# Performance work log

Measured on AMD Instinct MI355X. Metric: run time of the kernel, lower is better.

## Reference

```python
import jax, jax.numpy as jnp
import numpy as np

# model constants (match init_kwargs)
VOCAB = 32000
DIM = 1024
HEADS = 8
DH = DIM // HEADS
LAYERS = 2
K_SLOTS = 128
KR = 16   # read top-k
KW = 16   # write top-k
CHUNK = 256
GAMMA = 0.9  # slot memory decay per chunk


def setup_inputs() -> dict:
    key = jax.random.key(0)
    ks = jax.random.split(key, 12)
    B, S = 2, 4096
    s = 0.02
    inp = {
        "tokens": jax.random.randint(ks[0], (B, S), 0, VOCAB, dtype=jnp.int32),
        "embed": jax.random.normal(ks[1], (VOCAB, DIM), jnp.float32) * s,
        "Wq": jax.random.normal(ks[2], (LAYERS, DIM, DIM), jnp.float32) * s,
        "Wk": jax.random.normal(ks[3], (LAYERS, DIM, DIM), jnp.float32) * s,
        "Wv": jax.random.normal(ks[4], (LAYERS, DIM, DIM), jnp.float32) * s,
        "Wo": jax.random.normal(ks[5], (LAYERS, DIM, DIM), jnp.float32) * s,
        "slot_keys": jax.random.normal(ks[6], (LAYERS, HEADS, K_SLOTS, DH), jnp.float32) * s,
        "ln_g": jnp.ones((LAYERS, DIM), jnp.float32),
        "ln_b": jnp.zeros((LAYERS, DIM), jnp.float32),
        "fg": jnp.ones((DIM,), jnp.float32),
        "fb": jnp.zeros((DIM,), jnp.float32),
        "Wout": jax.random.normal(ks[7], (DIM, VOCAB), jnp.float32) * s,
        "bout": jnp.zeros((VOCAB,), jnp.float32),
    }
    return inp


def _layer_norm(x, g, b, eps=1e-5):
    mu = jnp.mean(x, axis=-1, keepdims=True)
    var = jnp.var(x, axis=-1, keepdims=True)
    return (x - mu) * jax.lax.rsqrt(var + eps) * g + b


def _mhdsra2_layer(x, M, Wq, Wk, Wv, Wo, sk, causal_mask):
    # x: [B,T,D], M: [B,H,K,dh] slot value memory, sk: [H,K,dh] slot keys
    B, T, D = x.shape
    H, K, dh = sk.shape
    scale = 1.0 / np.sqrt(dh)
    q = (x @ Wq).reshape(B, T, H, dh).transpose(0, 2, 1, 3)  # bhtd
    k = (x @ Wk).reshape(B, T, H, dh).transpose(0, 2, 1, 3)
    v = (x @ Wv).reshape(B, T, H, dh).transpose(0, 2, 1, 3)
    # --- slot READ: top-kr addressed gather from memory ---
    rs = jnp.einsum('bhtd,hkd->bhtk', q, sk) * scale           # [B,H,T,K]
    rv, ri = jax.lax.top_k(rs, KR)                              # [B,H,T,KR]
    rw = jax.nn.softmax(rv, axis=-1)
    gathered = jnp.take_along_axis(M[:, :, None, :, :], ri[..., None], axis=3)  # [B,H,T,KR,dh]
    read = jnp.einsum('bhtk,bhtkd->bhtd', rw, gathered)
    # --- local causal attention within chunk (local_window = chunk_size) ---
    att = jnp.einsum('bhtd,bhsd->bhts', q, k) * scale
    att = jnp.where(causal_mask, att, jnp.float32(-1e9))
    att = jax.nn.softmax(att, axis=-1)
    local = jnp.einsum('bhts,bhsd->bhtd', att, v)
    out = (local + read).transpose(0, 2, 1, 3).reshape(B, T, D) @ Wo
    # --- slot WRITE: top-kw addressed scatter into memory ---
    ws = jnp.einsum('bhtd,hkd->bhtk', k, sk) * scale
    wv_, wi = jax.lax.top_k(ws, KW)
    ww = jax.nn.softmax(wv_, axis=-1)                           # [B,H,T,KW]
    contrib = ww[..., None] * v[:, :, :, None, :]               # [B,H,T,KW,dh]
    bI = jnp.arange(B)[:, None, None, None]
    hI = jnp.arange(H)[None, :, None, None]
    delta = jnp.zeros_like(M).at[bI, hI, wi].add(contrib)
    M_next = GAMMA * M + delta
    return out, M_next


def reference(tokens, embed, Wq, Wk, Wv, Wo, slot_keys, ln_g, ln_b, fg, fb, Wout, bout):
    B, S = tokens.shape
    hidden = embed[tokens]                                      # [B,S,D]
    n_chunks = S // CHUNK
    chunks = hidden.reshape(B, n_chunks, CHUNK, DIM).transpose(1, 0, 2, 3)
    M0 = jnp.zeros((LAYERS, B, HEADS, K_SLOTS, DH), jnp.float32)
    causal_mask = jnp.tril(jnp.ones((CHUNK, CHUNK), bool))

    def body(M_all, chunk):
        new_Ms = []
        for l in range(LAYERS):
            residual = chunk
            xn = _layer_norm(chunk, ln_g[l], ln_b[l])
            out, Mn = _mhdsra2_layer(xn, M_all[l], Wq[l], Wk[l], Wv[l], Wo[l], slot_keys[l], causal_mask)
            new_Ms.append(jax.lax.stop_gradient(Mn))  # detach_state=True
            chunk = residual + out
        return jnp.stack(new_Ms), chunk

    _, outs = jax.lax.scan(body, M0, chunks)                    # [n_chunks,B,T,D]
    out = outs.transpose(1, 0, 2, 3).reshape(B, S, DIM)
    out = _layer_norm(out, fg, fb)
    return out @ Wout + bout                                     # [B,S,VOCAB]
```

## Files before the change

kernel.cpp:

```cpp
#include <hip/hip_runtime.h>

#define DIMM 1024
#define NHEADS 8
#define DH 128
#define NSLOTS 128
#define CHUNK 256
#define NCHUNK 16
#define NB 2
#define SEQ 4096
#define NROWS (NB * SEQ)
#define NVOCAB 32000
#define GAMMA64 0.9
#define SCALE64 0.08838834764831845
#define TAU 1e-6
#define MAXFLAG 65536

typedef unsigned short u16;
typedef __attribute__((ext_vector_type(4))) float f32x4;
typedef __attribute__((ext_vector_type(8))) short s16x8;

struct alignas(8) u16x4 { u16 x, y, z, w; };

__device__ __forceinline__ u16 f2bf(float f) {
  union { float f; unsigned u; } v; v.f = f;
  return (u16)((v.u + 0x7FFFu + ((v.u >> 16) & 1u)) >> 16);
}
__device__ __forceinline__ float bf2f(u16 u) {
  union { unsigned u; float f; } v; v.u = ((unsigned)u) << 16; return v.f;
}
__device__ __forceinline__ void split3s(float x, u16& h, u16& m, u16& l) {
  h = f2bf(x); float r = x - bf2f(h);
  m = f2bf(r); float r2 = r - bf2f(m);
  l = f2bf(r2);
}

__device__ __forceinline__ void gld16(void* lds, const void* g) {
  __builtin_amdgcn_global_load_lds(
      (const __attribute__((address_space(1))) unsigned*)g,
      (__attribute__((address_space(3))) unsigned*)lds, 16, 0, 0);
}
__device__ __forceinline__ f32x4 mfma16(s16x8 a, s16x8 b, f32x4 c) {
  return __builtin_amdgcn_mfma_f32_16x16x32_bf16(a, b, c, 0, 0, 0);
}

__global__ __launch_bounds__(256) void embed64_kernel(
    const int* __restrict__ tok, const float* __restrict__ emb,
    double* __restrict__ hid) {
  const int row = blockIdx.x;
  const int t = tok[row];
  const float4 v = ((const float4*)(emb + (size_t)t * DIMM))[threadIdx.x];
  double* o = hid + (size_t)row * DIMM + threadIdx.x * 4;
  o[0] = (double)v.x; o[1] = (double)v.y; o[2] = (double)v.z; o[3] = (double)v.w;
}

template <int MODE>
__global__ __launch_bounds__(256) void ln64_kernel(
    const double* __restrict__ x, const float* __restrict__ g,
    const float* __restrict__ bb, double* __restrict__ o64,
    u16* __restrict__ oh, u16* __restrict__ om, u16* __restrict__ ol) {
  const int row = blockIdx.x, tid = threadIdx.x;
  const double* xr = x + (size_t)row * DIMM + tid * 4;
  const double v0 = xr[0], v1 = xr[1], v2 = xr[2], v3 = xr[3];
  __shared__ double red[4];
  double s1 = v0 + v1 + v2 + v3;
#pragma unroll
  for (int off = 32; off >= 1; off >>= 1) s1 += __shfl_xor(s1, off);
  if ((tid & 63) == 0) red[tid >> 6] = s1;
  __syncthreads();
  const double mu = (red[0] + red[1] + red[2] + red[3]) * (1.0 / DIMM);
  __syncthreads();
  const double d0 = v0 - mu, d1 = v1 - mu, d2 = v2 - mu, d3 = v3 - mu;
  double s2 = d0 * d0 + d1 * d1 + d2 * d2 + d3 * d3;
#pragma unroll
  for (int off = 32; off >= 1; off >>= 1) s2 += __shfl_xor(s2, off);
  if ((tid & 63) == 0) red[tid >> 6] = s2;
  __syncthreads();
  const double var = (red[0] + red[1] + red[2] + red[3]) * (1.0 / DIMM);
  const double rs = 1.0 / sqrt(var + 1e-5);
  const float4 g4 = ((const float4*)g)[tid];
  const float4 b4 = ((const float4*)bb)[tid];
  const double y0 = d0 * rs * (double)g4.x + (double)b4.x;
  const double y1 = d1 * rs * (double)g4.y + (double)b4.y;
  const double y2 = d2 * rs * (double)g4.z + (double)b4.z;
  const double y3 = d3 * rs * (double)g4.w + (double)b4.w;
  if (MODE == 0) {
    double* o = o64 + (size_t)row * DIMM + tid * 4;
    o[0] = y0; o[1] = y1; o[2] = y2; o[3] = y3;
    u16x4 rh, rm, rl;
    split3s((float)y0, rh.x, rm.x, rl.x);
    split3s((float)y1, rh.y, rm.y, rl.y);
    split3s((float)y2, rh.z, rm.z, rl.z);
    split3s((float)y3, rh.w, rm.w, rl.w);
    ((u16x4*)(oh + (size_t)row * DIMM))[tid] = rh;
    ((u16x4*)(om + (size_t)row * DIMM))[tid] = rm;
    ((u16x4*)(ol + (size_t)row * DIMM))[tid] = rl;
  } else {
    u16x4 r;
    r.x = f2bf((float)y0); r.y = f2bf((float)y1);
    r.z = f2bf((float)y2); r.w = f2bf((float)y3);
    ((u16x4*)(oh + (size_t)row * DIMM))[tid] = r;
  }
}

__global__ void transconv3_kernel(const float* __restrict__ W,
                                  u16* __restrict__ WTh, u16* __restrict__ WTm,
                                  u16* __restrict__ WTl, int K, int N) {
  __shared__ float tile[32][33];
  const int n0 = blockIdx.x * 32, k0 = blockIdx.y * 32;
  const int tx = threadIdx.x, ty = threadIdx.y;
#pragma unroll
  for (int i = 0; i < 4; i++)
    tile[ty + 8 * i][tx] = W[(size_t)(k0 + ty + 8 * i) * N + n0 + tx];
  __syncthreads();
#pragma unroll
  for (int i = 0; i < 4; i++) {
    u16 h, m, l;
    split3s(tile[tx][ty + 8 * i], h, m, l);
    const size_t o = (size_t)(n0 + ty + 8 * i) * K + k0 + tx;
    WTh[o] = h; WTm[o] = m; WTl[o] = l;
  }
}

__global__ __launch_bounds__(256) void w2_kernel(const float* __restrict__ W,
                                                 const float* __restrict__ sk,
                                                 double* __restrict__ W2) {
  __shared__ float sksh[128];
  const int r = blockIdx.x, h = r >> 7;
  const int tid = threadIdx.x;
  if (tid < 128) sksh[tid] = sk[(size_t)r * DH + tid];
  __syncthreads();
  for (int d = tid; d < DIMM; d += 256) {
    const float* wrow = W + (size_t)d * DIMM + h * DH;
    double acc = 0.0;
#pragma unroll 8
    for (int j = 0; j < 128; j++) acc += (double)wrow[j] * (double)sksh[j];
    W2[(size_t)r * DIMM + d] = acc;
  }
}

template <bool RES, typename TC>
__global__ __launch_bounds__(256) void gemm3d_kernel(
    const u16* __restrict__ Ah, const u16* __restrict__ Am,
    const u16* __restrict__ Al, const u16* __restrict__ Bh,
    const u16* __restrict__ Bm, const u16* __restrict__ Bl,
    TC* __restrict__ C, const TC* __restrict__ Cres, int M, int N, int K) {
  __shared__ u16 lds[6 * 128 * 32];
  const int tid = threadIdx.x;
  const int bn = blockIdx.x, bm = blockIdx.y;
  const int wid = tid >> 6, lane = tid & 63;
  const int wr = (wid >> 1) * 64, wc = (wid & 1) * 64;
  f32x4 acc[4][4] = {};
  const int row0 = tid >> 2;
  const int colb = (tid & 3) << 4;
  const u16* Gs[6] = {Ah, Am, Al, Bh, Bm, Bl};
  const char* g0[6];
  const char* g1[6];
  char* lb[6];
#pragma unroll
  for (int i = 0; i < 6; i++) {
    const int rbase = (i < 3 ? bm : bn) * 128;
    g0[i] = (const char*)Gs[i] + ((size_t)(rbase + row0) * K) * 2 + colb;
    g1[i] = (const char*)Gs[i] + ((size_t)(rbase + row0 + 64) * K) * 2 + colb;
    lb[i] = (char*)lds + i * 8192 + (tid & 192) * 16;
  }
  const int fo = (lane & 15) * 64 + (lane >> 4) * 16;
  const char* paH = (const char*)lds + 0 + wr * 64 + fo;
  const char* paM = paH + 8192;
  const char* paL = paH + 16384;
  const char* pbH = (const char*)lds + 24576 + wc * 64 + fo;
  const char* pbM = pbH + 8192;
  const char* pbL = pbH + 16384;

  for (int k0 = 0; k0 < K; k0 += 32) {
    const size_t kb = (size_t)k0 * 2;
#pragma unroll
    for (int i = 0; i < 6; i++) {
      gld16(lb[i], g0[i] + kb);
      gld16(lb[i] + 4096, g1[i] + kb);
    }
    __syncthreads();
    s16x8 bh[4], bm_[4], bl[4];
#pragma unroll
    for (int n = 0; n < 4; n++) {
      bh[n] = *(const s16x8*)(pbH + n * 1024);
      bm_[n] = *(const s16x8*)(pbM + n * 1024);
      bl[n] = *(const s16x8*)(pbL + n * 1024);
    }
#pragma unroll
    for (int m = 0; m < 4; m++) {
      const s16x8 ah = *(const s16x8*)(paH + m * 1024);
      const s16x8 am = *(const s16x8*)(paM + m * 1024);
      const s16x8 al = *(const s16x8*)(paL + m * 1024);
#pragma unroll
      for (int n = 0; n < 4; n++) {
        f32x4 t = acc[m][n];
        t = mfma16(al, bh[n], t);
        t = mfma16(ah, bl[n], t);
        t = mfma16(am, bm_[n], t);
        t = mfma16(am, bh[n], t);
        t = mfma16(ah, bm_[n], t);
        t = mfma16(ah, bh[n], t);
        acc[m][n] = t;
      }
    }
    __syncthreads();
  }
#pragma unroll
  for (int m = 0; m < 4; m++)
#pragma unroll
    for (int n = 0; n < 4; n++)
#pragma unroll
      for (int j = 0; j < 4; j++) {
        const int r = bm * 128 + wr + m * 16 + (lane >> 4) * 4 + j;
        const int c = bn * 128 + wc + n * 16 + (lane & 15);
        TC v = (TC)acc[m][n][j];
        if (RES) v += Cres[(size_t)r * N + c];
        C[(size_t)r * N + c] = v;
      }
}

__global__ __launch_bounds__(256) void topk_flag_kernel(
    const float* __restrict__ Q, const float* __restrict__ K,
    const float* __restrict__ sk, int* __restrict__ riQ, int* __restrict__ riK,
    double* __restrict__ rwQ, double* __restrict__ rwK,
    int* __restrict__ fcnts, int* __restrict__ flq, int* __restrict__ flk) {
  __shared__ float vsh[4][130];
  const int which = blockIdx.y;
  const float* X = which ? K : Q;
  int* oidx = which ? riK : riQ;
  double* ow = which ? rwK : rwQ;
  int* fcnt = fcnts + which;
  int* flist = which ? flk : flq;
  const int wid = threadIdx.x >> 6, lane = threadIdx.x & 63;
  const int rid = blockIdx.x * 4 + wid;
  const int t = rid & 4095, h = (rid >> 12) & 7, b = rid >> 15;
  const float* xrow = X + ((size_t)b * SEQ + t) * DIMM + h * DH;
  vsh[wid][lane * 2] = xrow[lane * 2];
  vsh[wid][lane * 2 + 1] = xrow[lane * 2 + 1];
  const float* skh = sk + (size_t)h * NSLOTS * DH;
  double s0 = 0.0, s1 = 0.0;
#pragma unroll 8
  for (int d = 0; d < DH; d++) {
    const double v = (double)vsh[wid][d];
    s0 += v * (double)skh[(size_t)lane * DH + d];
    s1 += v * (double)skh[(size_t)(lane + 64) * DH + d];
  }
  s0 *= SCALE64; s1 *= SCALE64;
  double selv = -1e300; int seli = 0;
  double v0 = s0, v1 = s1;
  for (int it = 0; it < 17; it++) {
    double m; int mi;
    if (v1 > v0) { m = v1; mi = lane + 64; } else { m = v0; mi = lane; }
#pragma unroll
    for (int off = 1; off < 64; off <<= 1) {
      const double om = __shfl_xor(m, off);
      const int oi = __shfl_xor(mi, off);
      if (om > m || (om == m && oi < mi)) { m = om; mi = oi; }
    }
    if (lane == it) { selv = m; seli = mi; }
    if (mi == lane) v0 = -1e300;
    if (mi == lane + 64) v1 = -1e300;
  }
  const double mx = __shfl(selv, 0);
  const double v15 = __shfl(selv, 15);
  const double v16 = __shfl(selv, 16);
  if (lane == 0 && (v15 - v16) < TAU) {
    const int p = atomicAdd(fcnt, 1);
    if (p < MAXFLAG) flist[p] = rid;
  }
  const float e = (lane < 16) ? expf((float)(selv - mx)) : 0.0f;
  double ss = (double)e;
  ss += __shfl_xor(ss, 1); ss += __shfl_xor(ss, 2);
  ss += __shfl_xor(ss, 4); ss += __shfl_xor(ss, 8);
  if (lane < 16) {
    ow[(size_t)rid * 16 + lane] = (double)e / ss;
    oidx[(size_t)rid * 16 + lane] = seli;
  }
}

__global__ __launch_bounds__(256) void fixup_kernel(
    const int* __restrict__ fcnts, const int* __restrict__ flq,
    const int* __restrict__ flk, const double* __restrict__ xn,
    const double* __restrict__ W2q, const double* __restrict__ W2k,
    int* __restrict__ riQ, int* __restrict__ riK, double* __restrict__ rwQ,
    double* __restrict__ rwK) {
  __shared__ double xsh[1024];
  __shared__ double psh[256];
  __shared__ double ssh[128];
  const int which = blockIdx.y;
  const int* flist = which ? flk : flq;
  const double* W2 = which ? W2k : W2q;
  int* oidx = which ? riK : riQ;
  double* ow = which ? rwK : rwQ;
  const int tid = threadIdx.x;
  const int n = min(fcnts[which], MAXFLAG);
  for (int i = blockIdx.x; i < n; i += gridDim.x) {
    __syncthreads();
    const int rid = flist[i];
    const int t = rid & 4095, h = (rid >> 12) & 7, b = rid >> 15;
    const double* xr = xn + ((size_t)b * SEQ + t) * DIMM;
    for (int j = tid; j < DIMM; j += 256) xsh[j] = xr[j];
    __syncthreads();
    const int slot = tid >> 1, half = tid & 1;
    const double* w2r = W2 + (size_t)(h * NSLOTS + slot) * DIMM + half * 512;
    const double* xp = xsh + half * 512;
    double acc = 0.0;
#pragma unroll 8
    for (int d = 0; d < 512; d++) acc += xp[d] * w2r[d];
    psh[tid] = acc;
    __syncthreads();
    if (tid < 128) ssh[tid] = (psh[2 * tid] + psh[2 * tid + 1]) * SCALE64;
    __syncthreads();
    if (tid < 64) {
      const int lane = tid;
      double selv = -1e300; int seli = 0;
      double v0 = ssh[lane], v1 = ssh[lane + 64];
      for (int it = 0; it < 16; it++) {
        double m; int mi;
        if (v1 > v0) { m = v1; mi = lane + 64; } else { m = v0; mi = lane; }
#pragma unroll
        for (int off = 1; off < 64; off <<= 1) {
          const double om = __shfl_xor(m, off);
          const int oi = __shfl_xor(mi, off);
          if (om > m || (om == m && oi < mi)) { m = om; mi = oi; }
        }
        if (lane == it) { selv = m; seli = mi; }
        if (mi == lane) v0 = -1e300;
        if (mi == lane + 64) v1 = -1e300;
      }
      const double mx = __shfl(selv, 0);
      const float e = (lane < 16) ? expf((float)(selv - mx)) : 0.0f;
      double ss = (double)e;
      ss += __shfl_xor(ss, 1); ss += __shfl_xor(ss, 2);
      ss += __shfl_xor(ss, 4); ss += __shfl_xor(ss, 8);
      if (lane < 16) {
        ow[(size_t)rid * 16 + lane] = (double)e / ss;
        oidx[(size_t)rid * 16 + lane] = seli;
      }
    }
  }
}

__global__ __launch_bounds__(512) void delta64_kernel(
    const int* __restrict__ wi, const double* __restrict__ ww,
    const float* __restrict__ V, double* __restrict__ delta) {
  __shared__ short slot_sh[4096];
  __shared__ double w_sh[4096];
  __shared__ u16 list[4096];
  __shared__ int cnt[NSLOTS], off_[NSLOTS];
  const int bid = blockIdx.x;
  const int c = bid & 15, h = (bid >> 4) & 7, b = bid >> 7;
  const int tid = threadIdx.x;
  if (tid < NSLOTS) cnt[tid] = 0;
  __syncthreads();
  const size_t ebase = ((size_t)(b * 8 + h) * SEQ + (size_t)c * CHUNK) * 16;
#pragma unroll
  for (int i = 0; i < 8; i++) {
    const int e = tid + i * 512;
    const int s = wi[ebase + e];
    slot_sh[e] = (short)s;
    w_sh[e] = ww[ebase + e];
    atomicAdd(&cnt[s], 1);
  }
  __syncthreads();
  if (tid == 0) {
    int a = 0;
    for (int s = 0; s < NSLOTS; s++) { off_[s] = a; a += cnt[s]; }
  }
  __syncthreads();
  if (tid < NSLOTS) {
    int p = off_[tid];
    const short me = (short)tid;
    for (int e = 0; e < 4096; e++)
      if (slot_sh[e] == me) list[p++] = (u16)e;
  }
  __syncthreads();
  const int slot = tid >> 2, dbase = (tid & 3) * 32;
  double acc[32] = {};
  const int start = off_[slot], len = cnt[slot];
  const float* vbase =
      V + ((size_t)b * SEQ + (size_t)c * CHUNK) * DIMM + h * DH + dbase;
  for (int i = 0; i < len; i++) {
    const int e = list[start + i];
    const double w = w_sh[e];
    const float* vp = vbase + (size_t)(e >> 4) * DIMM;
#pragma unroll
    for (int d = 0; d < 32; d++) acc[d] += w * (double)vp[d];
  }
  double* dst = delta + ((size_t)bid * NSLOTS + slot) * DH + dbase;
#pragma unroll
  for (int d = 0; d < 32; d++) dst[d] = acc[d];
}

__global__ __launch_bounds__(256) void attn_fused(
    const float* __restrict__ Q, const float* __restrict__ Kb,
    const float* __restrict__ V, float* __restrict__ outb) {
  __shared__ float Qs[32][130];
  __shared__ float KVs[16][130];
  const int idx = blockIdx.x;
  const int rq = idx & 7, h = (idx >> 3) & 7, c = (idx >> 6) & 15, b = idx >> 10;
  const int tid = threadIdx.x;
  const size_t rowbase = (size_t)b * SEQ + (size_t)c * CHUNK;
  {
    const int r = tid >> 3, d0 = (tid & 7) * 16;
    const float* qp = Q + (rowbase + rq * 32 + r) * DIMM + h * DH + d0;
#pragma unroll
    for (int j = 0; j < 16; j++) Qs[r][d0 + j] = qp[j];
  }
  const int row = tid >> 3;
  const int sub = tid & 7;
  const int row_abs = rq * 32 + row;
  const int ntile = 2 * rq + 2;
  float pexp[16][2];
#pragma unroll
  for (int kt = 0; kt < 16; kt++) { pexp[kt][0] = -1e30f; pexp[kt][1] = -1e30f; }

#pragma unroll
  for (int kt = 0; kt < 16; kt++) {
    if (kt < ntile) {
      __syncthreads();
      {
        const int r = tid >> 4, d0 = (tid & 15) * 8;
        const float* kp = Kb + (rowbase + kt * 16 + r) * DIMM + h * DH + d0;
#pragma unroll
        for (int j = 0; j < 8; j++) KVs[r][d0 + j] = kp[j];
      }
      __syncthreads();
#pragma unroll
      for (int kk = 0; kk < 2; kk++) {
        const int key = sub * 2 + kk;
        double s = 0.0;
#pragma unroll 8
        for (int d = 0; d < DH; d++)
          s += (double)Qs[row][d] * (double)KVs[key][d];
        const int kabs = kt * 16 + key;
        pexp[kt][kk] = (kabs <= row_abs) ? (float)(s * SCALE64) : -1e30f;
      }
    }
  }
  float m = -1e30f;
#pragma unroll
  for (int kt = 0; kt < 16; kt++) {
    m = fmaxf(m, pexp[kt][0]); m = fmaxf(m, pexp[kt][1]);
  }
  m = fmaxf(m, __shfl_xor(m, 1));
  m = fmaxf(m, __shfl_xor(m, 2));
  m = fmaxf(m, __shfl_xor(m, 4));
  double ss = 0.0;
#pragma unroll
  for (int kt = 0; kt < 16; kt++) {
#pragma unroll
    for (int j = 0; j < 2; j++) {
      const float e = __expf(pexp[kt][j] - m);
      pexp[kt][j] = e;
      ss += (double)e;
    }
  }
  ss += __shfl_xor(ss, 1); ss += __shfl_xor(ss, 2); ss += __shfl_xor(ss, 4);
  const double inv = 1.0 / ss;
#pragma unroll
  for (int kt = 0; kt < 16; kt++) {
    pexp[kt][0] = (float)((double)pexp[kt][0] * inv);
    pexp[kt][1] = (float)((double)pexp[kt][1] * inv);
  }
  double acc[16] = {};
#pragma unroll
  for (int kt = 0; kt < 16; kt++) {
    if (kt < ntile) {
      __syncthreads();
      {
        const int r = tid >> 4, d0 = (tid & 15) * 8;
        const float* vp = V + (rowbase + kt * 16 + r) * DIMM + h * DH + d0;
#pragma unroll
        for (int j = 0; j < 8; j++) KVs[r][d0 + j] = vp[j];
      }
      __syncthreads();
#pragma unroll
      for (int key = 0; key < 16; key++) {
        const int src = (tid & 56) | (key >> 1);
        const float pf = __shfl(pexp[kt][key & 1], src, 64);
        const double pd = (double)pf;
        const float* vr = &KVs[key][sub * 16];
#pragma unroll
        for (int d = 0; d < 16; d++) acc[d] += pd * (double)vr[d];
      }
    }
  }
  float* op = outb + (rowbase + row_abs) * DIMM + h * DH + sub * 16;
#pragma unroll
  for (int d = 0; d < 16; d++) op[d] = (float)acc[d];
}

__global__ __launch_bounds__(256) void recur64_kernel(
    const int* __restrict__ ri, const double* __restrict__ rw,
    const double* __restrict__ delta, const float* __restrict__ inb,
    u16* __restrict__ sh, u16* __restrict__ sm, u16* __restrict__ sl) {
  __shared__ double Msh[NSLOTS][17];
  const int bid = blockIdx.x;
  const int ds = bid & 7, h = (bid >> 3) & 7, b = bid >> 6;
  const int tid = threadIdx.x;
  for (int i = tid; i < NSLOTS * 17; i += 256) ((double*)Msh)[i] = 0.0;
  __syncthreads();
  for (int c = 0; c < NCHUNK; c++) {
    const size_t rbase =
        ((size_t)(b * 8 + h) * SEQ + (size_t)c * CHUNK + tid) * 16;
    double a[16] = {};
#pragma unroll
    for (int j = 0; j < 16; j++) {
      const int slot = ri[rbase + j];
      const double w = rw[rbase + j];
      const double* mp = &Msh[slot][0];
#pragma unroll
      for (int d = 0; d < 16; d++) a[d] += w * mp[d];
    }
    const size_t base = ((size_t)b * SEQ + (size_t)c * CHUNK + tid) * DIMM +
                        h * DH + ds * 16;
    const float* ip = inb + base;
    u16x4 rh[4], rm[4], rl[4];
#pragma unroll
    for (int q = 0; q < 4; q++) {
      float f0 = (float)((double)ip[q * 4 + 0] + a[q * 4 + 0]);
      float f1 = (float)((double)ip[q * 4 + 1] + a[q * 4 + 1]);
      float f2 = (float)((double)ip[q * 4 + 2] + a[q * 4 + 2]);
      float f3 = (float)((double)ip[q * 4 + 3] + a[q * 4 + 3]);
      split3s(f0, rh[q].x, rm[q].x, rl[q].x);
      split3s(f1, rh[q].y, rm[q].y, rl[q].y);
      split3s(f2, rh[q].z, rm[q].z, rl[q].z);
      split3s(f3, rh[q].w, rm[q].w, rl[q].w);
    }
#pragma unroll
    for (int q = 0; q < 4; q++) {
      ((u16x4*)(sh + base))[q] = rh[q];
      ((u16x4*)(sm + base))[q] = rm[q];
      ((u16x4*)(sl + base))[q] = rl[q];
    }
    __syncthreads();
    const int slot = tid >> 1, d8 = (tid & 1) * 8;
    const double* dp = delta +
        (((size_t)(b * 8 + h) * NCHUNK + c) * NSLOTS + slot) * DH + ds * 16 + d8;
#pragma unroll
    for (int d = 0; d < 8; d++)
      Msh[slot][d8 + d] = GAMMA64 * Msh[slot][d8 + d] + dp[d];
    __syncthreads();
  }
}

__global__ void transconv_kernel(const float* __restrict__ W,
                                 u16* __restrict__ WT, int K, int N) {
  __shared__ float tile[32][33];
  const int n0 = blockIdx.x * 32, k0 = blockIdx.y * 32;
  const int tx = threadIdx.x, ty = threadIdx.y;
#pragma unroll
  for (int i = 0; i < 4; i++)
    tile[ty + 8 * i][tx] = W[(size_t)(k0 + ty + 8 * i) * N + n0 + tx];
  __syncthreads();
#pragma unroll
  for (int i = 0; i < 4; i++)
    WT[(size_t)(n0 + ty + 8 * i) * K + k0 + tx] = f2bf(tile[tx][ty + 8 * i]);
}

template <bool BIAS>
__global__ __launch_bounds__(256) void gemm_kernel(
    const u16* __restrict__ A, const u16* __restrict__ B, float* __restrict__ C,
    const float* __restrict__ bias, int M, int N, int K) {
  __shared__ u16 As[128 * 32];
  __shared__ u16 Bs[128 * 32];
  const int tid = threadIdx.x;
  const int lid = blockIdx.y * gridDim.x + blockIdx.x;
  const int npm = M / 128;
  const int ngrid = N / 128;
  const int GN = 16;
  const int ppg = GN * npm;
  const int gid = lid / ppg;
  const int first_n = gid * GN;
  const int gsz = min(GN, ngrid - first_n);
  const int local = lid - gid * ppg;
  const int bn = first_n + local % gsz;
  const int bm = local / gsz;
  const int wid = tid >> 6, lane = tid & 63;
  const int wr = (wid >> 1) * 64, wc = (wid & 1) * 64;
  f32x4 acc[4][4] = {};
  const int row0 = tid >> 2;
  const int colb = (tid & 3) << 4;
  const char* A0 = (const char*)A + ((size_t)(bm * 128 + row0) * K) * 2 + colb;
  const char* A1 = (const char*)A + ((size_t)(bm * 128 + row0 + 64) * K) * 2 + colb;
  const char* B0 = (const char*)B + ((size_t)(bn * 128 + row0) * K) * 2 + colb;
  const char* B1 = (const char*)B + ((size_t)(bn * 128 + row0 + 64) * K) * 2 + colb;
  char* lA0 = (char*)As + (tid & 192) * 16;
  char* lB0 = (char*)Bs + (tid & 192) * 16;
  const char* pa = (const char*)As + wr * 64 + (lane & 15) * 64 + (lane >> 4) * 16;
  const char* pb = (const char*)Bs + wc * 64 + (lane & 15) * 64 + (lane >> 4) * 16;
  for (int k0 = 0; k0 < K; k0 += 32) {
    const size_t kb = (size_t)k0 * 2;
    gld16(lA0, A0 + kb);
    gld16(lA0 + 4096, A1 + kb);
    gld16(lB0, B0 + kb);
    gld16(lB0 + 4096, B1 + kb);
    __syncthreads();
    s16x8 af[4], bf[4];
#pragma unroll
    for (int m = 0; m < 4; m++) af[m] = *(const s16x8*)(pa + m * 1024);
#pragma unroll
    for (int n = 0; n < 4; n++) bf[n] = *(const s16x8*)(pb + n * 1024);
#pragma unroll
    for (int m = 0; m < 4; m++)
#pragma unroll
      for (int n = 0; n < 4; n++) acc[m][n] = mfma16(af[m], bf[n], acc[m][n]);
    __syncthreads();
  }
#pragma unroll
  for (int m = 0; m < 4; m++)
#pragma unroll
    for (int n = 0; n < 4; n++)
#pragma unroll
      for (int j = 0; j < 4; j++) {
        const int r = bm * 128 + wr + m * 16 + (lane >> 4) * 4 + j;
        const int c = bn * 128 + wc + n * 16 + (lane & 15);
        float v = acc[m][n][j];
        if (BIAS) v += bias[c];
        C[(size_t)r * N + c] = v;
      }
}

extern "C" void kernel_launch(void* const* d_in, const int* in_sizes, int n_in,
                              void* d_out, int out_size, void* d_ws,
                              size_t ws_size, hipStream_t stream) {
  (void)in_sizes; (void)n_in; (void)out_size; (void)ws_size;
  const int* tokens = (const int*)d_in[0];
  const float* embed = (const float*)d_in[1];
  const float* Wq = (const float*)d_in[2];
  const float* Wk = (const float*)d_in[3];
  const float* Wv = (const float*)d_in[4];
  const float* Wo = (const float*)d_in[5];
  const float* slot_keys = (const float*)d_in[6];
  const float* ln_g = (const float*)d_in[7];
  const float* ln_b = (const float*)d_in[8];
  const float* fg = (const float*)d_in[9];
  const float* fb = (const float*)d_in[10];
  const float* Wout = (const float*)d_in[11];
  const float* bout = (const float*)d_in[12];
  float* out = (float*)d_out;

  char* p = (char*)d_ws;
  auto alloc = [&](size_t bytes) -> char* {
    char* r = p;
    p += (bytes + 255) & ~(size_t)255;
    return r;
  };
  const size_t RD = (size_t)NROWS * DIMM;
  double* hidden64 = (double*)alloc(RD * 8);
  double* xn64 = (double*)alloc(RD * 8);
  float* q32 = (float*)alloc(RD * 4);
  float* k32 = (float*)alloc(RD * 4);
  float* v32 = (float*)alloc(RD * 4);
  float* local32 = (float*)alloc(RD * 4);
  double* delta64 =
      (double*)alloc((size_t)NB * NHEADS * NCHUNK * NSLOTS * DH * 8);
  int* ri = (int*)alloc((size_t)65536 * 16 * 4);
  int* wi = (int*)alloc((size_t)65536 * 16 * 4);
  double* rw64 = (double*)alloc((size_t)65536 * 16 * 8);
  double* ww64 = (double*)alloc((size_t)65536 * 16 * 8);
  u16* sAh = (u16*)alloc(RD * 2);
  u16* sAm = (u16*)alloc(RD * 2);
  u16* sAl = (u16*)alloc(RD * 2);
  u16* WTh = (u16*)alloc((size_t)8 * DIMM * DIMM * 2);
  u16* WTm = (u16*)alloc((size_t)8 * DIMM * DIMM * 2);
  u16* WTl = (u16*)alloc((size_t)8 * DIMM * DIMM * 2);
  double* W2q = (double*)alloc((size_t)2 * DIMM * DIMM * 8);
  double* W2k = (double*)alloc((size_t)2 * DIMM * DIMM * 8);
  u16* WoutT = (u16*)alloc((size_t)NVOCAB * DIMM * 2);
  int* fcnts = (int*)alloc(256);
  int* flq = (int*)alloc((size_t)MAXFLAG * 4);
  int* flk = (int*)alloc((size_t)MAXFLAG * 4);

  u16* xnb = (u16*)q32;

  const float* Wmats[4] = {Wq, Wk, Wv, Wo};
  for (int l = 0; l < 2; l++) {
    for (int w = 0; w < 4; w++) {
      const size_t o = ((size_t)l * 4 + w) * DIMM * DIMM;
      transconv3_kernel<<<dim3(DIMM / 32, DIMM / 32), dim3(32, 8), 0, stream>>>(
          Wmats[w] + (size_t)l * DIMM * DIMM, WTh + o, WTm + o, WTl + o, DIMM,
          DIMM);
    }
    const float* skl = slot_keys + (size_t)l * NHEADS * NSLOTS * DH;
    w2_kernel<<<1024, 256, 0, stream>>>(Wq + (size_t)l * DIMM * DIMM, skl,
                                        W2q + (size_t)l * DIMM * DIMM);
    w2_kernel<<<1024, 256, 0, stream>>>(Wk + (size_t)l * DIMM * DIMM, skl,
                                        W2k + (size_t)l * DIMM * DIMM);
  }

  embed64_kernel<<<NROWS, 256, 0, stream>>>(tokens, embed, hidden64);

  const dim3 g3(DIMM / 128, NROWS / 128);
  for (int l = 0; l < 2; l++) {
    const size_t oq = ((size_t)l * 4 + 0) * DIMM * DIMM;
    const size_t ok = ((size_t)l * 4 + 1) * DIMM * DIMM;
    const size_t ov = ((size_t)l * 4 + 2) * DIMM * DIMM;
    const size_t oo = ((size_t)l * 4 + 3) * DIMM * DIMM;
    ln64_kernel<0><<<NROWS, 256, 0, stream>>>(hidden64, ln_g + l * DIMM,
                                              ln_b + l * DIMM, xn64, sAh, sAm,
                                              sAl);
    gemm3d_kernel<false, float><<<g3, 256, 0, stream>>>(
        sAh, sAm, sAl, WTh + oq, WTm + oq, WTl + oq, q32, nullptr, NROWS, DIMM,
        DIMM);
    gemm3d_kernel<false, float><<<g3, 256, 0, stream>>>(
        sAh, sAm, sAl, WTh + ok, WTm + ok, WTl + ok, k32, nullptr, NROWS, DIMM,
        DIMM);
    gemm3d_kernel<false, float><<<g3, 256, 0, stream>>>(
        sAh, sAm, sAl, WTh + ov, WTm + ov, WTl + ov, v32, nullptr, NROWS, DIMM,
        DIMM);
    const float* skl = slot_keys + (size_t)l * NHEADS * NSLOTS * DH;
    hipMemsetAsync(fcnts, 0, 8, stream);
    topk_flag_kernel<<<dim3(16384, 2), 256, 0, stream>>>(
        q32, k32, skl, ri, wi, rw64, ww64, fcnts, flq, flk);
    fixup_kernel<<<dim3(512, 2), 256, 0, stream>>>(
        fcnts, flq, flk, xn64, W2q + (size_t)l * DIMM * DIMM,
        W2k + (size_t)l * DIMM * DIMM, ri, wi, rw64, ww64);
    delta64_kernel<<<NB * NHEADS * NCHUNK, 512, 0, stream>>>(wi, ww64, v32,
                                                             delta64);
    attn_fused<<<NB * NCHUNK * NHEADS * 8, 256, 0, stream>>>(q32, k32, v32,
                                                             local32);
    recur64_kernel<<<NB * NHEADS * 8, 256, 0, stream>>>(ri, rw64, delta64,
                                                        local32, sAh, sAm,
                                                        sAl);
    gemm3d_kernel<true, double><<<g3, 256, 0, stream>>>(
        sAh, sAm, sAl, WTh + oo, WTm + oo, WTl + oo, hidden64, hidden64, NROWS,
        DIMM, DIMM);
  }
  transconv_kernel<<<dim3(NVOCAB / 32, DIMM / 32), dim3(32, 8), 0, stream>>>(
      Wout, WoutT, DIMM, NVOCAB);
  ln64_kernel<1><<<NROWS, 256, 0, stream>>>(hidden64, fg, fb, nullptr, xnb,
                                            nullptr, nullptr);
  gemm_kernel<true><<<dim3(NVOCAB / 128, NROWS / 128), 256, 0, stream>>>(
      xnb, WoutT, out, bout, NROWS, NVOCAB, DIMM);
}
```

Before: 6.314 ms.

## Compute slot scores with split-bf16 MFMA GEMM and separate top-k selection

The per-row fp64 dot-product scoring in the top-k kernel is replaced by a tiled matrix-core GEMM. Q and K are split into three bf16 parts, giving near-fp32 accuracy from six MFMA products per tile. Scores go to an fp32 buffer and a new select kernel does the top-k in float instead of double. This removes slow fp64 FMA work but adds conversion kernels, a 64MB score buffer round-trip and slightly lower score precision. Tie cases are still sent to the existing fixup kernel.

```diff
diff --git a/kernel.cpp b/kernel.cpp
--- a/kernel.cpp
+++ b/kernel.cpp
@@ -12,7 +12,7 @@
 #define NVOCAB 32000
 #define GAMMA64 0.9
 #define SCALE64 0.08838834764831845
-#define TAU 1e-6
+#define TAU 1e-6f
 #define MAXFLAG 65536
 
 typedef unsigned short u16;
@@ -121,6 +121,17 @@
   }
 }
 
+__global__ __launch_bounds__(256) void cvt3_32_kernel(
+    const float* __restrict__ in, u16* __restrict__ oh, u16* __restrict__ om,
+    u16* __restrict__ ol) {
+  const size_t i = (size_t)blockIdx.x * 256 + threadIdx.x;
+  const float4 v = ((const float4*)in)[i];
+  u16x4 rh, rm, rl;
+  split3s(v.x, rh.x, rm.x, rl.x); split3s(v.y, rh.y, rm.y, rl.y);
+  split3s(v.z, rh.z, rm.z, rl.z); split3s(v.w, rh.w, rm.w, rl.w);
+  ((u16x4*)oh)[i] = rh; ((u16x4*)om)[i] = rm; ((u16x4*)ol)[i] = rl;
+}
+
 __global__ __launch_bounds__(256) void w2_kernel(const float* __restrict__ W,
                                                  const float* __restrict__ sk,
                                                  double* __restrict__ W2) {
@@ -219,56 +230,135 @@
       }
 }
 
-__global__ __launch_bounds__(256) void topk_flag_kernel(
-    const float* __restrict__ Q, const float* __restrict__ K,
-    const float* __restrict__ sk, int* __restrict__ riQ, int* __restrict__ riK,
+__global__ __launch_bounds__(256) void score3_kernel(
+    const u16* __restrict__ Qh, const u16* __restrict__ Qm,
+    const u16* __restrict__ Ql, const u16* __restrict__ Kh3,
+    const u16* __restrict__ Km3, const u16* __restrict__ Kl3,
+    const u16* __restrict__ skh, const u16* __restrict__ skm,
+    const u16* __restrict__ skl, float* __restrict__ S) {
+  __shared__ u16 lds[6 * 128 * 32];
+  const int tid = threadIdx.x;
+  const int bm = blockIdx.x;
+  const int y = blockIdx.y;
+  const int which = y >> 4, b = (y >> 3) & 1, h = y & 7;
+  const u16* Ah = which ? Kh3 : Qh;
+  const u16* Am = which ? Km3 : Qm;
+  const u16* Al = which ? Kl3 : Ql;
+  const int wid = tid >> 6, lane = tid & 63;
+  const int wr = (wid >> 1) * 64, wc = (wid & 1) * 64;
+  f32x4 acc[4][4] = {};
+  const int row0 = tid >> 2;
+  const int colb = (tid & 3) << 4;
+  const size_t arow = (size_t)(b * SEQ + bm * 128);
+  const u16* Gs[6] = {Ah, Am, Al, skh, skm, skl};
+  const char* g0[6];
+  const char* g1[6];
+  char* lb[6];
+#pragma unroll
+  for (int i = 0; i < 6; i++) {
+    if (i < 3) {
+      g0[i] = (const char*)Gs[i] + (arow + row0) * 2048 + h * 256 + colb;
+      g1[i] = (const char*)Gs[i] + (arow + row0 + 64) * 2048 + h * 256 + colb;
+    } else {
+      g0[i] = (const char*)Gs[i] + ((size_t)h * 128 + row0) * 256 + colb;
+      g1[i] = (const char*)Gs[i] + ((size_t)h * 128 + row0 + 64) * 256 + colb;
+    }
+    lb[i] = (char*)lds + i * 8192 + (tid & 192) * 16;
+  }
+  const int fo = (lane & 15) * 64 + (lane >> 4) * 16;
+  const char* paH = (const char*)lds + 0 + wr * 64 + fo;
+  const char* paM = paH + 8192;
+  const char* paL = paH + 16384;
+  const char* pbH = (const char*)lds + 24576 + wc * 64 + fo;
+  const char* pbM = pbH + 8192;
+  const char* pbL = pbH + 16384;
+
+  for (int k0 = 0; k0 < DH; k0 += 32) {
+    const size_t kb = (size_t)k0 * 2;
+#pragma unroll
+    for (int i = 0; i < 6; i++) {
+      gld16(lb[i], g0[i] + kb);
+      gld16(lb[i] + 4096, g1[i] + kb);
+    }
+    __syncthreads();
+    s16x8 bh[4], bm_[4], bl[4];
+#pragma unroll
+    for (int n = 0; n < 4; n++) {
+      bh[n] = *(const s16x8*)(pbH + n * 1024);
+      bm_[n] = *(const s16x8*)(pbM + n * 1024);
+      bl[n] = *(const s16x8*)(pbL + n * 1024);
+    }
+#pragma unroll
+    for (int m = 0; m < 4; m++) {
+      const s16x8 ah = *(const s16x8*)(paH + m * 1024);
+      const s16x8 am = *(const s16x8*)(paM + m * 1024);
+      const s16x8 al = *(const s16x8*)(paL + m * 1024);
+#pragma unroll
+      for (int n = 0; n < 4; n++) {
+        f32x4 t = acc[m][n];
+        t = mfma16(al, bh[n], t);
+        t = mfma16(ah, bl[n], t);
+        t = mfma16(am, bm_[n], t);
+        t = mfma16(am, bh[n], t);
+        t = mfma16(ah, bm_[n], t);
+        t = mfma16(ah, bh[n], t);
+        acc[m][n] = t;
+      }
+    }
+    __syncthreads();
+  }
+  const size_t sbase =
+      (size_t)which * 65536 + (size_t)(b * 8 + h) * 4096 + (size_t)bm * 128;
+#pragma unroll
+  for (int m = 0; m < 4; m++)
+#pragma unroll
+    for (int n = 0; n < 4; n++)
+#pragma unroll
+      for (int j = 0; j < 4; j++) {
+        const int r = wr + m * 16 + (lane >> 4) * 4 + j;
+        const int c = wc + n * 16 + (lane & 15);
+        S[(sbase + r) * NSLOTS + c] = acc[m][n][j];
+      }
+}
+
+__global__ __launch_bounds__(256) void select_kernel(
+    const float* __restrict__ S, int* __restrict__ riQ, int* __restrict__ riK,
     double* __restrict__ rwQ, double* __restrict__ rwK,
     int* __restrict__ fcnts, int* __restrict__ flq, int* __restrict__ flk) {
-  __shared__ float vsh[4][130];
   const int which = blockIdx.y;
-  const float* X = which ? K : Q;
   int* oidx = which ? riK : riQ;
   double* ow = which ? rwK : rwQ;
   int* fcnt = fcnts + which;
   int* flist = which ? flk : flq;
   const int wid = threadIdx.x >> 6, lane = threadIdx.x & 63;
   const int rid = blockIdx.x * 4 + wid;
-  const int t = rid & 4095, h = (rid >> 12) & 7, b = rid >> 15;
-  const float* xrow = X + ((size_t)b * SEQ + t) * DIMM + h * DH;
-  vsh[wid][lane * 2] = xrow[lane * 2];
-  vsh[wid][lane * 2 + 1] = xrow[lane * 2 + 1];
-  const float* skh = sk + (size_t)h * NSLOTS * DH;
-  double s0 = 0.0, s1 = 0.0;
-#pragma unroll 8
-  for (int d = 0; d < DH; d++) {
-    const double v = (double)vsh[wid][d];
-    s0 += v * (double)skh[(size_t)lane * DH + d];
-    s1 += v * (double)skh[(size_t)(lane + 64) * DH + d];
-  }
-  s0 *= SCALE64; s1 *= SCALE64;
-  double selv = -1e300; int seli = 0;
-  double v0 = s0, v1 = s1;
+  const float2 sv =
+      *(const float2*)(S + ((size_t)which * 65536 + rid) * NSLOTS + lane * 2);
+  const float sc = (float)SCALE64;
+  float v0 = sv.x * sc, v1 = sv.y * sc;
+  const int i0 = lane * 2, i1 = lane * 2 + 1;
+  float selv = -1e30f; int seli = 0;
   for (int it = 0; it < 17; it++) {
-    double m; int mi;
-    if (v1 > v0) { m = v1; mi = lane + 64; } else { m = v0; mi = lane; }
+    float m; int mi;
+    if (v1 > v0) { m = v1; mi = i1; } else { m = v0; mi = i0; }
 #pragma unroll
     for (int off = 1; off < 64; off <<= 1) {
-      const double om = __shfl_xor(m, off);
+      const float om = __shfl_xor(m, off);
       const int oi = __shfl_xor(mi, off);
       if (om > m || (om == m && oi < mi)) { m = om; mi = oi; }
     }
     if (lane == it) { selv = m; seli = mi; }
-    if (mi == lane) v0 = -1e300;
-    if (mi == lane + 64) v1 = -1e300;
-  }
-  const double mx = __shfl(selv, 0);
-  const double v15 = __shfl(selv, 15);
-  const double v16 = __shfl(selv, 16);
+    if (mi == i0) v0 = -1e30f;
+    if (mi == i1) v1 = -1e30f;
+  }
+  const float mx = __shfl(selv, 0);
+  const float v15 = __shfl(selv, 15);
+  const float v16 = __shfl(selv, 16);
   if (lane == 0 && (v15 - v16) < TAU) {
     const int p = atomicAdd(fcnt, 1);
     if (p < MAXFLAG) flist[p] = rid;
   }
-  const float e = (lane < 16) ? expf((float)(selv - mx)) : 0.0f;
+  const float e = (lane < 16) ? expf(selv - mx) : 0.0f;
   double ss = (double)e;
   ss += __shfl_xor(ss, 1); ss += __shfl_xor(ss, 2);
   ss += __shfl_xor(ss, 4); ss += __shfl_xor(ss, 8);
@@ -663,17 +753,25 @@
   u16* sAh = (u16*)alloc(RD * 2);
   u16* sAm = (u16*)alloc(RD * 2);
   u16* sAl = (u16*)alloc(RD * 2);
+  u16* kBh = (u16*)alloc(RD * 2);
+  u16* kBm = (u16*)alloc(RD * 2);
+  u16* kBl = (u16*)alloc(RD * 2);
   u16* WTh = (u16*)alloc((size_t)8 * DIMM * DIMM * 2);
   u16* WTm = (u16*)alloc((size_t)8 * DIMM * DIMM * 2);
   u16* WTl = (u16*)alloc((size_t)8 * DIMM * DIMM * 2);
   double* W2q = (double*)alloc((size_t)2 * DIMM * DIMM * 8);
   double* W2k = (double*)alloc((size_t)2 * DIMM * DIMM * 8);
-  u16* WoutT = (u16*)alloc((size_t)NVOCAB * DIMM * 2);
+  const size_t SKE = (size_t)2 * NHEADS * NSLOTS * DH;
+  u16* sk3h = (u16*)alloc(SKE * 2);
+  u16* sk3m = (u16*)alloc(SKE * 2);
+  u16* sk3l = (u16*)alloc(SKE * 2);
+  float* S = (float*)alloc((size_t)2 * 65536 * NSLOTS * 4);
   int* fcnts = (int*)alloc(256);
   int* flq = (int*)alloc((size_t)MAXFLAG * 4);
   int* flk = (int*)alloc((size_t)MAXFLAG * 4);
 
   u16* xnb = (u16*)q32;
+  u16* WoutT = (u16*)k32;
 
   const float* Wmats[4] = {Wq, Wk, Wv, Wo};
   for (int l = 0; l < 2; l++) {
@@ -689,6 +787,7 @@
     w2_kernel<<<1024, 256, 0, stream>>>(Wk + (size_t)l * DIMM * DIMM, skl,
                                         W2k + (size_t)l * DIMM * DIMM);
   }
+  cvt3_32_kernel<<<SKE / 1024, 256, 0, stream>>>(slot_keys, sk3h, sk3m, sk3l);
 
   embed64_kernel<<<NROWS, 256, 0, stream>>>(tokens, embed, hidden64);
 
@@ -698,6 +797,7 @@
     const size_t ok = ((size_t)l * 4 + 1) * DIMM * DIMM;
     const size_t ov = ((size_t)l * 4 + 2) * DIMM * DIMM;
     const size_t oo = ((size_t)l * 4 + 3) * DIMM * DIMM;
+    const size_t sko = (size_t)l * NHEADS * NSLOTS * DH;
     ln64_kernel<0><<<NROWS, 256, 0, stream>>>(hidden64, ln_g + l * DIMM,
                                               ln_b + l * DIMM, xn64, sAh, sAm,
                                               sAl);
@@ -710,10 +810,13 @@
     gemm3d_kernel<false, float><<<g3, 256, 0, stream>>>(
         sAh, sAm, sAl, WTh + ov, WTm + ov, WTl + ov, v32, nullptr, NROWS, DIMM,
         DIMM);
-    const float* skl = slot_keys + (size_t)l * NHEADS * NSLOTS * DH;
+    cvt3_32_kernel<<<RD / 1024, 256, 0, stream>>>(q32, sAh, sAm, sAl);
+    cvt3_32_kernel<<<RD / 1024, 256, 0, stream>>>(k32, kBh, kBm, kBl);
     hipMemsetAsync(fcnts, 0, 8, stream);
-    topk_flag_kernel<<<dim3(16384, 2), 256, 0, stream>>>(
-        q32, k32, skl, ri, wi, rw64, ww64, fcnts, flq, flk);
+    score3_kernel<<<dim3(32, 32), 256, 0, stream>>>(
+        sAh, sAm, sAl, kBh, kBm, kBl, sk3h + sko, sk3m + sko, sk3l + sko, S);
+    select_kernel<<<dim3(16384, 2), 256, 0, stream>>>(S, ri, wi, rw64, ww64,
+                                                      fcnts, flq, flk);
     fixup_kernel<<<dim3(512, 2), 256, 0, stream>>>(
         fcnts, flq, flk, xn64, W2q + (size_t)l * DIMM * DIMM,
         W2k + (size_t)l * DIMM * DIMM, ri, wi, rw64, ww64);
```

Result: faster. 5.222 ms (-17.3%).
